# Kernel optimization log

Measured on AMD Instinct MI355X. Metric: run time of the kernel, lower is better.

The kernel has to match this reference:

```python
import jax, jax.numpy as jnp
import numpy as np

EMB = 1024
HID = 1024

def setup_inputs() -> dict:
    key = jax.random.key(0)
    k1, k2, k3, k4, k5 = jax.random.split(key, 5)
    s_ih = 1.0 / np.sqrt(HID)
    embeds = jax.random.normal(k1, (64, 512, EMB), dtype=jnp.float32)
    W_ih = jax.random.uniform(k2, (HID, EMB), jnp.float32, -s_ih, s_ih)
    W_hh = jax.random.uniform(k3, (HID, HID), jnp.float32, -s_ih, s_ih)
    b_ih = jax.random.uniform(k4, (HID,), jnp.float32, -s_ih, s_ih)
    b_hh = jax.random.uniform(k5, (HID,), jnp.float32, -s_ih, s_ih)
    return {"embeds": embeds, "W_ih": W_ih, "W_hh": W_hh, "b_ih": b_ih, "b_hh": b_hh}

def reference(embeds, W_ih, W_hh, b_ih, b_hh):
    # Elman RNN with tanh: h_t = tanh(x_t W_ih^T + b_ih + h_{t-1} W_hh^T + b_hh)
    B, S, _ = embeds.shape
    # Precompute input projection for all timesteps in one big GEMM: (B,S,H)
    x_proj = jnp.einsum('bse,he->bsh', embeds, W_ih) + b_ih + b_hh
    h0 = jnp.zeros((B, W_hh.shape[0]), dtype=embeds.dtype)

    def step(h, xp_t):
        h_new = jnp.tanh(xp_t + h @ W_hh.T)
        return h_new, h_new

    # scan over time axis: inputs (S,B,H)
    _, hs = jax.lax.scan(step, h0, jnp.swapaxes(x_proj, 0, 1))
    return hs  # (S, B, H): hidden state at each timestep
```

## Files before the change

kernel.cpp:

```cpp
#include <hip/hip_runtime.h>
#include <math.h>

#define EMB   1024
#define HID   1024
#define BATCH   64
#define SEQ    512

#define NBG    16
#define BTILE   4
#define NJT    16
#define JTILE  64

#define SLOT  65536

typedef float f32x4 __attribute__((ext_vector_type(4)));

__global__ __launch_bounds__(256) void xproj_gemm(
    const float* __restrict__ A,
    const float* __restrict__ W,
    const float* __restrict__ b_ih,
    const float* __restrict__ b_hh,
    float* __restrict__ out)
{
    __shared__ float As[16][68];
    __shared__ float Ws[16][68];

    const int tid = threadIdx.x;
    const int tx  = tid & 15;
    const int ty  = tid >> 4;
    const int m0  = blockIdx.y * 64;
    const int n0  = blockIdx.x * 64;
    const int lrow = tid >> 2;
    const int lk   = (tid & 3) * 4;

    float acc[4][4] = {};

    for (int kt = 0; kt < EMB; kt += 16) {
        float4 av = *(const float4*)&A[(size_t)(m0 + lrow) * EMB + kt + lk];
        float4 wv = *(const float4*)&W[(size_t)(n0 + lrow) * EMB + kt + lk];
        As[lk + 0][lrow] = av.x; As[lk + 1][lrow] = av.y;
        As[lk + 2][lrow] = av.z; As[lk + 3][lrow] = av.w;
        Ws[lk + 0][lrow] = wv.x; Ws[lk + 1][lrow] = wv.y;
        Ws[lk + 2][lrow] = wv.z; Ws[lk + 3][lrow] = wv.w;
        __syncthreads();
        #pragma unroll
        for (int kk = 0; kk < 16; ++kk) {
            float4 a = *(const float4*)&As[kk][ty * 4];
            float4 w = *(const float4*)&Ws[kk][tx * 4];
            acc[0][0] += a.x * w.x; acc[0][1] += a.x * w.y;
            acc[0][2] += a.x * w.z; acc[0][3] += a.x * w.w;
            acc[1][0] += a.y * w.x; acc[1][1] += a.y * w.y;
            acc[1][2] += a.y * w.z; acc[1][3] += a.y * w.w;
            acc[2][0] += a.z * w.x; acc[2][1] += a.z * w.y;
            acc[2][2] += a.z * w.z; acc[2][3] += a.z * w.w;
            acc[3][0] += a.w * w.x; acc[3][1] += a.w * w.y;
            acc[3][2] += a.w * w.z; acc[3][3] += a.w * w.w;
        }
        __syncthreads();
    }

    const int n = n0 + tx * 4;
    float bias[4];
    #pragma unroll
    for (int j = 0; j < 4; ++j) bias[j] = b_ih[n + j] + b_hh[n + j];

    #pragma unroll
    for (int i = 0; i < 4; ++i) {
        const int m = m0 + ty * 4 + i;
        const int b = m >> 9;
        const int s = m & 511;
        float4 o;
        o.x = acc[i][0] + bias[0];
        o.y = acc[i][1] + bias[1];
        o.z = acc[i][2] + bias[2];
        o.w = acc[i][3] + bias[3];
        *(float4*)&out[((size_t)(s * 64 + b) << 10) + n] = o;
    }
}

__device__ __forceinline__ float red16(float x) {
    int xi, yi;
    xi = __builtin_bit_cast(int, x);
    yi = __builtin_amdgcn_update_dpp(0, xi, 0xB1, 0xF, 0xF, true);
    x += __builtin_bit_cast(float, yi);
    xi = __builtin_bit_cast(int, x);
    yi = __builtin_amdgcn_update_dpp(0, xi, 0x4E, 0xF, 0xF, true);
    x += __builtin_bit_cast(float, yi);
    xi = __builtin_bit_cast(int, x);
    yi = __builtin_amdgcn_update_dpp(0, xi, 0x124, 0xF, 0xF, true);
    x += __builtin_bit_cast(float, yi);
    xi = __builtin_bit_cast(int, x);
    yi = __builtin_amdgcn_update_dpp(0, xi, 0x128, 0xF, 0xF, true);
    x += __builtin_bit_cast(float, yi);
    return x;
}

__device__ __forceinline__ f32x4 llc_load4_sync(const float* p) {
    f32x4 v;
    asm volatile("global_load_dwordx4 %0, %1, off sc1\n\t"
                 "s_waitcnt vmcnt(0)"
                 : "=&v"(v) : "v"(p) : "memory");
    return v;
}

__device__ __forceinline__ void llc_load4x2_sync(const float* p0, const float* p1,
                                                 f32x4& a, f32x4& b) {
    asm volatile("global_load_dwordx4 %0, %2, off sc1\n\t"
                 "global_load_dwordx4 %1, %3, off sc1\n\t"
                 "s_waitcnt vmcnt(0)"
                 : "=&v"(a), "=&v"(b) : "v"(p0), "v"(p1) : "memory");
}

__device__ __forceinline__ bool inrange4(f32x4 v, float lo, float hi) {
    return v.x >= lo && v.x <= hi && v.y >= lo && v.y <= hi &&
           v.z >= lo && v.z <= hi && v.w >= lo && v.w <= hi;
}

__global__ __launch_bounds__(512, 2) void rnn_persist(
    const float* __restrict__ Whh,
    float* __restrict__ out,
    float* __restrict__ exch)
{
    const int tid  = threadIdx.x;
    const int wave = tid >> 6;
    const int lane = tid & 63;
    const int c    = lane & 15;
    const int jp   = (lane >> 4) & 3;
    const int jt   = blockIdx.x;
    const int bg   = blockIdx.y;
    const int jbase = jt * JTILE + wave * 8 + jp * 2;
    const int k0    = c * 64;

    f32x4 wr0[16], wr1[16];
    #pragma unroll
    for (int kq = 0; kq < 16; ++kq) {
        wr0[kq] = *(const f32x4*)&Whh[(size_t)jbase * HID + k0 + kq * 4];
        wr1[kq] = *(const f32x4*)&Whh[(size_t)(jbase + 1) * HID + k0 + kq * 4];
    }
    #pragma unroll
    for (int kq = 0; kq < 16; ++kq) {
        asm volatile("" : "+v"(wr0[kq]));
        asm volatile("" : "+v"(wr1[kq]));
    }

    __shared__ float hsf[2 * 4352];

    const int p0 = tid, p1 = tid + 512;
    const int b0i = p0 >> 8, r0 = p0 & 255;
    const int b1i = p1 >> 8, r1 = p1 & 255;
    const int exoff0 = (bg * BTILE + b0i) * HID + r0 * 4;
    const int exoff1 = (bg * BTILE + b1i) * HID + r1 * 4;
    const int ldo0 = b0i * 1088 + (r0 >> 4) * 68 + (r0 & 15) * 4;
    const int ldo1 = b1i * 1088 + (r1 >> 4) * 68 + (r1 & 15) * 4;

    const int ob   = c >> 1;
    const int oidx = (bg * BTILE + ob) * HID + (jbase + (c & 1));

    if (c < 8) {
        float h0 = tanhf(out[oidx]);
        out[oidx] = h0;
        __hip_atomic_store(&exch[oidx], h0, __ATOMIC_RELAXED,
                           __HIP_MEMORY_SCOPE_AGENT);
    }

    for (int t = 1; t < SEQ; ++t) {
        float* cur = out + (size_t)t * (BATCH * HID);

        float xp = 0.f;
        if (c < 8) xp = cur[oidx];

        const float off = 4.0f * (float)((t - 1) & 3);
        const float lo  = off - 1.0f, hi = off + 1.0f;
        const float* eb = exch + ((t - 1) & 1) * SLOT;

        f32x4 v0, v1;
        llc_load4x2_sync(eb + exoff0, eb + exoff1, v0, v1);
        bool ok0 = inrange4(v0, lo, hi);
        bool ok1 = inrange4(v1, lo, hi);
        while (!__all(ok0 && ok1)) {
            __builtin_amdgcn_s_sleep(1);
            if (!ok0) { v0 = llc_load4_sync(eb + exoff0); ok0 = inrange4(v0, lo, hi); }
            if (!ok1) { v1 = llc_load4_sync(eb + exoff1); ok1 = inrange4(v1, lo, hi); }
        }
        v0 -= off;
        v1 -= off;

        const int bufb = (t & 1) * 4352;
        *(f32x4*)&hsf[bufb + ldo0] = v0;
        *(f32x4*)&hsf[bufb + ldo1] = v1;
        __syncthreads();

        float acc[4][2];
        #pragma unroll
        for (int b = 0; b < 4; ++b) {
            const f32x4* hb = (const f32x4*)&hsf[bufb + b * 1088 + c * 68];
            f32x4 s0 = {0.f, 0.f, 0.f, 0.f};
            f32x4 s1 = {0.f, 0.f, 0.f, 0.f};
            #pragma unroll
            for (int kq = 0; kq < 16; ++kq) {
                f32x4 h4 = hb[kq];
                s0 += h4 * wr0[kq];
                s1 += h4 * wr1[kq];
            }
            acc[b][0] = (s0.x + s0.y) + (s0.z + s0.w);
            acc[b][1] = (s1.x + s1.y) + (s1.z + s1.w);
        }

        #pragma unroll
        for (int b = 0; b < 4; ++b) {
            acc[b][0] = red16(acc[b][0]);
            acc[b][1] = red16(acc[b][1]);
        }

        float vb0 = (c & 1) ? acc[0][1] : acc[0][0];
        float vb1 = (c & 1) ? acc[1][1] : acc[1][0];
        float vb2 = (c & 1) ? acc[2][1] : acc[2][0];
        float vb3 = (c & 1) ? acc[3][1] : acc[3][0];
        float vlo = (c & 2) ? vb1 : vb0;
        float vhi = (c & 2) ? vb3 : vb2;
        float v   = (c & 4) ? vhi : vlo;
        if (c < 8) {
            float hv = tanhf(xp + v);
            cur[oidx] = hv;
            __hip_atomic_store(&exch[(t & 1) * SLOT + oidx],
                               hv + 4.0f * (float)(t & 3),
                               __ATOMIC_RELAXED, __HIP_MEMORY_SCOPE_AGENT);
        }
    }
}

extern "C" void kernel_launch(void* const* d_in, const int* in_sizes, int n_in,
                              void* d_out, int out_size, void* d_ws, size_t ws_size,
                              hipStream_t stream) {
    const float* embeds = (const float*)d_in[0];
    const float* W_ih   = (const float*)d_in[1];
    const float* W_hh   = (const float*)d_in[2];
    const float* b_ih   = (const float*)d_in[3];
    const float* b_hh   = (const float*)d_in[4];
    float* out = (float*)d_out;

    (void)in_sizes; (void)n_in; (void)out_size; (void)ws_size;

    hipMemsetAsync(d_ws, 0x7F, 2 * SLOT * sizeof(float), stream);

    dim3 gA(HID / 64, (BATCH * SEQ) / 64);
    xproj_gemm<<<gA, 256, 0, stream>>>(embeds, W_ih, b_ih, b_hh, out);

    dim3 gR(NJT, NBG);
    rnn_persist<<<gR, 512, 0, stream>>>(W_hh, out, (float*)d_ws);
}
```

Before: 2.574 ms.

## Pipeline RNN step per batch row with async prefetch of next hidden slice

The persistent RNN kernel now walks the four batch rows of each tile one at a time instead of gathering the whole 4x1024 hidden block before computing. Each row is published to the exchange buffer as soon as its tanh is done, one iteration late. The next row's exchange slice is prefetched asynchronously, so polling, compute and publishing overlap across batch rows and the critical cross-block dependency chain gets shorter. In exchange there are four barriers per timestep instead of one, and the ordering relies on hand-written waitcnt and barrier assembly. The final row of the last step is written out after the loop.

```diff
diff --git a/kernel.cpp b/kernel.cpp
--- a/kernel.cpp
+++ b/kernel.cpp
@@ -1,17 +1,18 @@
 #include <hip/hip_runtime.h>
 #include <math.h>
 
-#define EMB   1024
-#define HID   1024
-#define BATCH   64
-#define SEQ    512
-
-#define NBG    16
-#define BTILE   4
-#define NJT    16
-#define JTILE  64
-
-#define SLOT  65536
+#define EMB    1024
+#define HID    1024
+#define BATCH    64
+#define SEQ     512
+
+#define NBG     16
+#define BTILE    4
+#define NJT     16
+#define JTILE   64
+
+#define SLOT   65536
+#define STEPSZ 65536
 
 typedef float f32x4 __attribute__((ext_vector_type(4)));
 
@@ -95,6 +96,13 @@
     return x;
 }
 
+__device__ __forceinline__ f32x4 llc_load4_async(const float* p) {
+    f32x4 v;
+    asm volatile("global_load_dwordx4 %0, %1, off sc1"
+                 : "=&v"(v) : "v"(p) : "memory");
+    return v;
+}
+
 __device__ __forceinline__ f32x4 llc_load4_sync(const float* p) {
     f32x4 v;
     asm volatile("global_load_dwordx4 %0, %1, off sc1\n\t"
@@ -103,12 +111,13 @@
     return v;
 }
 
-__device__ __forceinline__ void llc_load4x2_sync(const float* p0, const float* p1,
-                                                 f32x4& a, f32x4& b) {
-    asm volatile("global_load_dwordx4 %0, %2, off sc1\n\t"
-                 "global_load_dwordx4 %1, %3, off sc1\n\t"
-                 "s_waitcnt vmcnt(0)"
-                 : "=&v"(a), "=&v"(b) : "v"(p0), "v"(p1) : "memory");
+__device__ __forceinline__ void wait_vm0() {
+    asm volatile("s_waitcnt vmcnt(0)" ::: "memory");
+    __builtin_amdgcn_sched_barrier(0);
+}
+
+__device__ __forceinline__ void bar_lgkm() {
+    asm volatile("s_waitcnt lgkmcnt(0)\n\ts_barrier" ::: "memory");
 }
 
 __device__ __forceinline__ bool inrange4(f32x4 v, float lo, float hi) {
@@ -125,10 +134,9 @@
     const int wave = tid >> 6;
     const int lane = tid & 63;
     const int c    = lane & 15;
-    const int jp   = (lane >> 4) & 3;
     const int jt   = blockIdx.x;
     const int bg   = blockIdx.y;
-    const int jbase = jt * JTILE + wave * 8 + jp * 2;
+    const int jbase = jt * JTILE + wave * 8 + ((lane >> 4) & 3) * 2;
     const int k0    = c * 64;
 
     f32x4 wr0[16], wr1[16];
@@ -143,89 +151,106 @@
         asm volatile("" : "+v"(wr1[kq]));
     }
 
-    __shared__ float hsf[2 * 4352];
-
-    const int p0 = tid, p1 = tid + 512;
-    const int b0i = p0 >> 8, r0 = p0 & 255;
-    const int b1i = p1 >> 8, r1 = p1 & 255;
-    const int exoff0 = (bg * BTILE + b0i) * HID + r0 * 4;
-    const int exoff1 = (bg * BTILE + b1i) * HID + r1 * 4;
-    const int ldo0 = b0i * 1088 + (r0 >> 4) * 68 + (r0 & 15) * 4;
-    const int ldo1 = b1i * 1088 + (r1 >> 4) * 68 + (r1 & 15) * 4;
-
-    const int ob   = c >> 1;
-    const int oidx = (bg * BTILE + ob) * HID + (jbase + (c & 1));
+    __shared__ float hsf[2 * 1088];
+
+    const bool have  = (tid < 256);
+    const int  fidx  = tid & 255;
+    const int  ldoff = (fidx >> 4) * 68 + (fidx & 15) * 4;
+    const int  gq    = fidx * 4;
+
+    const int jout  = jbase + (c & 1);
+    const int mybat = c >> 1;
+    const int orow  = (bg * BTILE + mybat) * HID + jout;
 
     if (c < 8) {
-        float h0 = tanhf(out[oidx]);
-        out[oidx] = h0;
-        __hip_atomic_store(&exch[oidx], h0, __ATOMIC_RELAXED,
+        float h0 = tanhf(out[orow]);
+        out[orow] = h0;
+        __hip_atomic_store(&exch[orow], h0, __ATOMIC_RELAXED,
                            __HIP_MEMORY_SCOPE_AGENT);
     }
 
+    float xp = 0.f;
+    if (c < 8) xp = out[(size_t)STEPSZ + orow];
+
+    f32x4 pf = {0.f, 0.f, 0.f, 0.f};
+    if (have) pf = llc_load4_async(exch + (bg * BTILE + 0) * HID + gq);
+
+    float pend = 0.f;
+
     for (int t = 1; t < SEQ; ++t) {
-        float* cur = out + (size_t)t * (BATCH * HID);
-
-        float xp = 0.f;
-        if (c < 8) xp = cur[oidx];
-
-        const float off = 4.0f * (float)((t - 1) & 3);
-        const float lo  = off - 1.0f, hi = off + 1.0f;
-        const float* eb = exch + ((t - 1) & 1) * SLOT;
-
-        f32x4 v0, v1;
-        llc_load4x2_sync(eb + exoff0, eb + exoff1, v0, v1);
-        bool ok0 = inrange4(v0, lo, hi);
-        bool ok1 = inrange4(v1, lo, hi);
-        while (!__all(ok0 && ok1)) {
-            __builtin_amdgcn_s_sleep(1);
-            if (!ok0) { v0 = llc_load4_sync(eb + exoff0); ok0 = inrange4(v0, lo, hi); }
-            if (!ok1) { v1 = llc_load4_sync(eb + exoff1); ok1 = inrange4(v1, lo, hi); }
-        }
-        v0 -= off;
-        v1 -= off;
-
-        const int bufb = (t & 1) * 4352;
-        *(f32x4*)&hsf[bufb + ldo0] = v0;
-        *(f32x4*)&hsf[bufb + ldo1] = v1;
-        __syncthreads();
-
-        float acc[4][2];
         #pragma unroll
         for (int b = 0; b < 4; ++b) {
-            const f32x4* hb = (const f32x4*)&hsf[bufb + b * 1088 + c * 68];
-            f32x4 s0 = {0.f, 0.f, 0.f, 0.f};
-            f32x4 s1 = {0.f, 0.f, 0.f, 0.f};
-            #pragma unroll
-            for (int kq = 0; kq < 16; ++kq) {
-                f32x4 h4 = hb[kq];
-                s0 += h4 * wr0[kq];
-                s1 += h4 * wr1[kq];
-            }
-            acc[b][0] = (s0.x + s0.y) + (s0.z + s0.w);
-            acc[b][1] = (s1.x + s1.y) + (s1.z + s1.w);
+            const int   tp    = t - 1;
+            const float off   = 4.0f * (float)(tp & 3);
+            const float lo    = off - 1.0f, hi = off + 1.0f;
+            const float* ebase = exch + (tp & 1) * SLOT + (bg * BTILE + b) * HID;
+
+            wait_vm0();
+
+            {
+                const int bprev = (b == 0) ? 3 : (b - 1);
+                const int tprev = (b == 0) ? (t - 1) : t;
+                if (!(b == 0 && t == 1)) {
+                    if (mybat == bprev) {
+                        const int oi = (bg * BTILE + bprev) * HID + jout;
+                        out[(size_t)tprev * STEPSZ + oi] = pend;
+                        __hip_atomic_store(&exch[(tprev & 1) * SLOT + oi],
+                                           pend + 4.0f * (float)(tprev & 3),
+                                           __ATOMIC_RELAXED,
+                                           __HIP_MEMORY_SCOPE_AGENT);
+                    }
+                }
+            }
+
+            bool ok = !have || inrange4(pf, lo, hi);
+            while (!__all(ok)) {
+                if (!ok) {
+                    pf = llc_load4_sync(ebase + gq);
+                    ok = inrange4(pf, lo, hi);
+                }
+            }
+
+            if (have) *(f32x4*)&hsf[(b & 1) * 1088 + ldoff] = pf - off;
+
+            {
+                const int bn = (b + 1) & 3;
+                const int tn = (b == 3) ? (t + 1) : t;
+                if (tn < SEQ) {
+                    const float* nb =
+                        exch + ((tn - 1) & 1) * SLOT + (bg * BTILE + bn) * HID;
+                    if (have) pf = llc_load4_async(nb + gq);
+                }
+            }
+
+            bar_lgkm();
+
+            {
+                const float* base = &hsf[(b & 1) * 1088 + c * 68];
+                f32x4 s0 = {0.f, 0.f, 0.f, 0.f};
+                f32x4 s1 = {0.f, 0.f, 0.f, 0.f};
+                #pragma unroll
+                for (int kq = 0; kq < 16; ++kq) {
+                    f32x4 h4 = *(const f32x4*)&base[kq * 4];
+                    s0 += h4 * wr0[kq];
+                    s1 += h4 * wr1[kq];
+                }
+                float a0 = (s0.x + s0.y) + (s0.z + s0.w);
+                float a1 = (s1.x + s1.y) + (s1.z + s1.w);
+                a0 = red16(a0);
+                a1 = red16(a1);
+                if (mybat == b) {
+                    pend = tanhf(xp + ((c & 1) ? a1 : a0));
+                }
+            }
+
+            if (b == 3 && t + 1 < SEQ) {
+                if (c < 8) xp = out[(size_t)(t + 1) * STEPSZ + orow];
+            }
         }
-
-        #pragma unroll
-        for (int b = 0; b < 4; ++b) {
-            acc[b][0] = red16(acc[b][0]);
-            acc[b][1] = red16(acc[b][1]);
-        }
-
-        float vb0 = (c & 1) ? acc[0][1] : acc[0][0];
-        float vb1 = (c & 1) ? acc[1][1] : acc[1][0];
-        float vb2 = (c & 1) ? acc[2][1] : acc[2][0];
-        float vb3 = (c & 1) ? acc[3][1] : acc[3][0];
-        float vlo = (c & 2) ? vb1 : vb0;
-        float vhi = (c & 2) ? vb3 : vb2;
-        float v   = (c & 4) ? vhi : vlo;
-        if (c < 8) {
-            float hv = tanhf(xp + v);
-            cur[oidx] = hv;
-            __hip_atomic_store(&exch[(t & 1) * SLOT + oidx],
-                               hv + 4.0f * (float)(t & 3),
-                               __ATOMIC_RELAXED, __HIP_MEMORY_SCOPE_AGENT);
-        }
+    }
+
+    if (mybat == 3) {
+        out[(size_t)(SEQ - 1) * STEPSZ + (bg * BTILE + 3) * HID + jout] = pend;
     }
 }
 
```

New measurement: 2.571 ms. Within noise of the previous version (-0.1%).

## Fuse input projection GEMM into persistent RNN kernel, overlapping with recurrence

Applied to the files above, without the earlier changes.

Removes the separate x-projection GEMM launch. Each persistent block now computes its own slice of the input projection: it precomputes the first 32 timesteps up front, then does one 64-wide K chunk per recurrent step to produce later timesteps ahead of use. The goal is to hide the GEMM work inside the latency-bound recurrence, where the block would otherwise idle waiting on the cross-block exchange. The cost is extra shared memory (about 70KB more per block), more instructions per step, and extra loads issued on the critical path.

```diff
diff --git a/kernel.cpp b/kernel.cpp
--- a/kernel.cpp
+++ b/kernel.cpp
@@ -1,82 +1,21 @@
 #include <hip/hip_runtime.h>
 #include <math.h>
 
-#define EMB   1024
-#define HID   1024
-#define BATCH   64
-#define SEQ    512
-
-#define NBG    16
-#define BTILE   4
-#define NJT    16
-#define JTILE  64
-
-#define SLOT  65536
+#define EMB    1024
+#define HID    1024
+#define BATCH    64
+#define SEQ     512
+
+#define NBG     16
+#define BTILE    4
+#define NJT     16
+#define JTILE   64
+
+#define SLOT   65536
+#define STEPSZ 65536
 
 typedef float f32x4 __attribute__((ext_vector_type(4)));
-
-__global__ __launch_bounds__(256) void xproj_gemm(
-    const float* __restrict__ A,
-    const float* __restrict__ W,
-    const float* __restrict__ b_ih,
-    const float* __restrict__ b_hh,
-    float* __restrict__ out)
-{
-    __shared__ float As[16][68];
-    __shared__ float Ws[16][68];
-
-    const int tid = threadIdx.x;
-    const int tx  = tid & 15;
-    const int ty  = tid >> 4;
-    const int m0  = blockIdx.y * 64;
-    const int n0  = blockIdx.x * 64;
-    const int lrow = tid >> 2;
-    const int lk   = (tid & 3) * 4;
-
-    float acc[4][4] = {};
-
-    for (int kt = 0; kt < EMB; kt += 16) {
-        float4 av = *(const float4*)&A[(size_t)(m0 + lrow) * EMB + kt + lk];
-        float4 wv = *(const float4*)&W[(size_t)(n0 + lrow) * EMB + kt + lk];
-        As[lk + 0][lrow] = av.x; As[lk + 1][lrow] = av.y;
-        As[lk + 2][lrow] = av.z; As[lk + 3][lrow] = av.w;
-        Ws[lk + 0][lrow] = wv.x; Ws[lk + 1][lrow] = wv.y;
-        Ws[lk + 2][lrow] = wv.z; Ws[lk + 3][lrow] = wv.w;
-        __syncthreads();
-        #pragma unroll
-        for (int kk = 0; kk < 16; ++kk) {
-            float4 a = *(const float4*)&As[kk][ty * 4];
-            float4 w = *(const float4*)&Ws[kk][tx * 4];
-            acc[0][0] += a.x * w.x; acc[0][1] += a.x * w.y;
-            acc[0][2] += a.x * w.z; acc[0][3] += a.x * w.w;
-            acc[1][0] += a.y * w.x; acc[1][1] += a.y * w.y;
-            acc[1][2] += a.y * w.z; acc[1][3] += a.y * w.w;
-            acc[2][0] += a.z * w.x; acc[2][1] += a.z * w.y;
-            acc[2][2] += a.z * w.z; acc[2][3] += a.z * w.w;
-            acc[3][0] += a.w * w.x; acc[3][1] += a.w * w.y;
-            acc[3][2] += a.w * w.z; acc[3][3] += a.w * w.w;
-        }
-        __syncthreads();
-    }
-
-    const int n = n0 + tx * 4;
-    float bias[4];
-    #pragma unroll
-    for (int j = 0; j < 4; ++j) bias[j] = b_ih[n + j] + b_hh[n + j];
-
-    #pragma unroll
-    for (int i = 0; i < 4; ++i) {
-        const int m = m0 + ty * 4 + i;
-        const int b = m >> 9;
-        const int s = m & 511;
-        float4 o;
-        o.x = acc[i][0] + bias[0];
-        o.y = acc[i][1] + bias[1];
-        o.z = acc[i][2] + bias[2];
-        o.w = acc[i][3] + bias[3];
-        *(float4*)&out[((size_t)(s * 64 + b) << 10) + n] = o;
-    }
-}
+typedef float f32x2 __attribute__((ext_vector_type(2)));
 
 __device__ __forceinline__ float red16(float x) {
     int xi, yi;
@@ -102,7 +41,6 @@
                  : "=&v"(v) : "v"(p) : "memory");
     return v;
 }
-
 __device__ __forceinline__ void llc_load4x2_sync(const float* p0, const float* p1,
                                                  f32x4& a, f32x4& b) {
     asm volatile("global_load_dwordx4 %0, %2, off sc1\n\t"
@@ -110,14 +48,17 @@
                  "s_waitcnt vmcnt(0)"
                  : "=&v"(a), "=&v"(b) : "v"(p0), "v"(p1) : "memory");
 }
-
 __device__ __forceinline__ bool inrange4(f32x4 v, float lo, float hi) {
     return v.x >= lo && v.x <= hi && v.y >= lo && v.y <= hi &&
            v.z >= lo && v.z <= hi && v.w >= lo && v.w <= hi;
 }
 
-__global__ __launch_bounds__(512, 2) void rnn_persist(
+__global__ __launch_bounds__(512, 2) void rnn_fused(
+    const float* __restrict__ embeds,
+    const float* __restrict__ W_ih,
     const float* __restrict__ Whh,
+    const float* __restrict__ b_ih,
+    const float* __restrict__ b_hh,
     float* __restrict__ out,
     float* __restrict__ exch)
 {
@@ -125,10 +66,9 @@
     const int wave = tid >> 6;
     const int lane = tid & 63;
     const int c    = lane & 15;
-    const int jp   = (lane >> 4) & 3;
     const int jt   = blockIdx.x;
     const int bg   = blockIdx.y;
-    const int jbase = jt * JTILE + wave * 8 + jp * 2;
+    const int jbase = jt * JTILE + wave * 8 + ((lane >> 4) & 3) * 2;
     const int k0    = c * 64;
 
     f32x4 wr0[16], wr1[16];
@@ -144,35 +84,106 @@
     }
 
     __shared__ float hsf[2 * 4352];
-
-    const int p0 = tid, p1 = tid + 512;
-    const int b0i = p0 >> 8, r0 = p0 & 255;
-    const int b1i = p1 >> 8, r1 = p1 & 255;
+    __shared__ float Axs[2][64][68];
+    __shared__ float Wxs[2][64][68];
+
+    const int b0i = tid >> 8,         r0 = tid & 255;
+    const int b1i = (tid + 512) >> 8, r1 = (tid + 512) & 255;
     const int exoff0 = (bg * BTILE + b0i) * HID + r0 * 4;
     const int exoff1 = (bg * BTILE + b1i) * HID + r1 * 4;
     const int ldo0 = b0i * 1088 + (r0 >> 4) * 68 + (r0 & 15) * 4;
     const int ldo1 = b1i * 1088 + (r1 >> 4) * 68 + (r1 & 15) * 4;
 
-    const int ob   = c >> 1;
-    const int oidx = (bg * BTILE + ob) * HID + (jbase + (c & 1));
+    const int jout  = jbase + (c & 1);
+    const int mybat = c >> 1;
+    const int orow  = (bg * BTILE + mybat) * HID + jout;
+
+    const int gty = tid >> 5;
+    const int gtx = tid & 31;
+    const int jx0 = jt * 64 + gtx * 2;
+    const float bias0 = b_ih[jx0] + b_hh[jx0];
+    const float bias1 = b_ih[jx0 + 1] + b_hh[jx0 + 1];
+    const int fm0 = (2 * tid) >> 4,     fk0 = (2 * tid) & 15;
+    const int fm1 = (2 * tid + 1) >> 4, fk1 = (2 * tid + 1) & 15;
+
+    f32x4 xaccA = {0.f,0.f,0.f,0.f};
+    f32x4 xaccB = {0.f,0.f,0.f,0.f};
+
+    auto xp_write = [&](int buf, f32x4 av0, f32x4 wv0, f32x4 av1, f32x4 wv1) {
+        Axs[buf][fk0*4+0][fm0]=av0.x; Axs[buf][fk0*4+1][fm0]=av0.y;
+        Axs[buf][fk0*4+2][fm0]=av0.z; Axs[buf][fk0*4+3][fm0]=av0.w;
+        Wxs[buf][fk0*4+0][fm0]=wv0.x; Wxs[buf][fk0*4+1][fm0]=wv0.y;
+        Wxs[buf][fk0*4+2][fm0]=wv0.z; Wxs[buf][fk0*4+3][fm0]=wv0.w;
+        Axs[buf][fk1*4+0][fm1]=av1.x; Axs[buf][fk1*4+1][fm1]=av1.y;
+        Axs[buf][fk1*4+2][fm1]=av1.z; Axs[buf][fk1*4+3][fm1]=av1.w;
+        Wxs[buf][fk1*4+0][fm1]=wv1.x; Wxs[buf][fk1*4+1][fm1]=wv1.y;
+        Wxs[buf][fk1*4+2][fm1]=wv1.z; Wxs[buf][fk1*4+3][fm1]=wv1.w;
+    };
+    auto xp_lda = [&](int sbase, int kc, int fm, int fk) -> f32x4 {
+        return *(const f32x4*)&embeds[
+            ((size_t)((bg*4 + (fm & 3)) * 512 + sbase + (fm >> 2)) << 10) + kc + fk*4];
+    };
+    auto xp_ldw = [&](int kc, int fm, int fk) -> f32x4 {
+        return *(const f32x4*)&W_ih[((size_t)(jt*64 + fm) << 10) + kc + fk*4];
+    };
+    auto xp_compute = [&](int buf) {
+        #pragma unroll
+        for (int kk = 0; kk < 64; ++kk) {
+            f32x4 a4 = *(const f32x4*)&Axs[buf][kk][gty * 4];
+            f32x2 w2 = *(const f32x2*)&Wxs[buf][kk][gtx * 2];
+            xaccA += a4 * w2.x;
+            xaccB += a4 * w2.y;
+        }
+    };
+    auto xp_store = [&](int sbase) {
+        float* o = &out[((size_t)((sbase + gty) * 64 + bg * 4) << 10) + jx0];
+        *(f32x2*)(o +    0) = f32x2{xaccA.x + bias0, xaccB.x + bias1};
+        *(f32x2*)(o + 1024) = f32x2{xaccA.y + bias0, xaccB.y + bias1};
+        *(f32x2*)(o + 2048) = f32x2{xaccA.z + bias0, xaccB.z + bias1};
+        *(f32x2*)(o + 3072) = f32x2{xaccA.w + bias0, xaccB.w + bias1};
+        xaccA = f32x4{0.f,0.f,0.f,0.f};
+        xaccB = f32x4{0.f,0.f,0.f,0.f};
+    };
+
+    for (int q = 0; q < 32; ++q) {
+        const int sb = (q >> 4) << 4;
+        const int kc = (q & 15) << 6;
+        xp_write(q & 1, xp_lda(sb, kc, fm0, fk0), xp_ldw(kc, fm0, fk0),
+                        xp_lda(sb, kc, fm1, fk1), xp_ldw(kc, fm1, fk1));
+        __syncthreads();
+        xp_compute(q & 1);
+        if ((q & 15) == 15) xp_store(sb);
+    }
+    __syncthreads();
 
     if (c < 8) {
-        float h0 = tanhf(out[oidx]);
-        out[oidx] = h0;
-        __hip_atomic_store(&exch[oidx], h0, __ATOMIC_RELAXED,
+        float h0 = tanhf(out[orow]);
+        out[orow] = h0;
+        __hip_atomic_store(&exch[orow], h0, __ATOMIC_RELAXED,
                            __HIP_MEMORY_SCOPE_AGENT);
     }
 
     for (int t = 1; t < SEQ; ++t) {
-        float* cur = out + (size_t)t * (BATCH * HID);
+        float* cur = out + (size_t)t * STEPSZ;
 
         float xp = 0.f;
-        if (c < 8) xp = cur[oidx];
+        if (c < 8) xp = cur[orow];
+
+        const bool doxp = (t <= 480);
+        const int  q    = t - 1;
+        const int  xbuf = q & 1;
+        const int  sb   = 32 + (q & ~15);
+        const int  kc   = (q & 15) << 6;
+        f32x4 av0, wv0, av1, wv1;
+        if (doxp) {
+            av0 = xp_lda(sb, kc, fm0, fk0); wv0 = xp_ldw(kc, fm0, fk0);
+            av1 = xp_lda(sb, kc, fm1, fk1); wv1 = xp_ldw(kc, fm1, fk1);
+            __builtin_amdgcn_sched_barrier(0);
+        }
 
         const float off = 4.0f * (float)((t - 1) & 3);
         const float lo  = off - 1.0f, hi = off + 1.0f;
         const float* eb = exch + ((t - 1) & 1) * SLOT;
-
         f32x4 v0, v1;
         llc_load4x2_sync(eb + exoff0, eb + exoff1, v0, v1);
         bool ok0 = inrange4(v0, lo, hi);
@@ -188,14 +199,14 @@
         const int bufb = (t & 1) * 4352;
         *(f32x4*)&hsf[bufb + ldo0] = v0;
         *(f32x4*)&hsf[bufb + ldo1] = v1;
+        if (doxp) xp_write(xbuf, av0, wv0, av1, wv1);
         __syncthreads();
 
         float acc[4][2];
         #pragma unroll
         for (int b = 0; b < 4; ++b) {
             const f32x4* hb = (const f32x4*)&hsf[bufb + b * 1088 + c * 68];
-            f32x4 s0 = {0.f, 0.f, 0.f, 0.f};
-            f32x4 s1 = {0.f, 0.f, 0.f, 0.f};
+            f32x4 s0 = {0.f,0.f,0.f,0.f}, s1 = {0.f,0.f,0.f,0.f};
             #pragma unroll
             for (int kq = 0; kq < 16; ++kq) {
                 f32x4 h4 = hb[kq];
@@ -205,13 +216,11 @@
             acc[b][0] = (s0.x + s0.y) + (s0.z + s0.w);
             acc[b][1] = (s1.x + s1.y) + (s1.z + s1.w);
         }
-
         #pragma unroll
         for (int b = 0; b < 4; ++b) {
             acc[b][0] = red16(acc[b][0]);
             acc[b][1] = red16(acc[b][1]);
         }
-
         float vb0 = (c & 1) ? acc[0][1] : acc[0][0];
         float vb1 = (c & 1) ? acc[1][1] : acc[1][0];
         float vb2 = (c & 1) ? acc[2][1] : acc[2][0];
@@ -221,10 +230,15 @@
         float v   = (c & 4) ? vhi : vlo;
         if (c < 8) {
             float hv = tanhf(xp + v);
-            cur[oidx] = hv;
-            __hip_atomic_store(&exch[(t & 1) * SLOT + oidx],
+            cur[orow] = hv;
+            __hip_atomic_store(&exch[(t & 1) * SLOT + orow],
                                hv + 4.0f * (float)(t & 3),
                                __ATOMIC_RELAXED, __HIP_MEMORY_SCOPE_AGENT);
+        }
+
+        if (doxp) {
+            xp_compute(xbuf);
+            if ((t & 15) == 0) xp_store(sb);
         }
     }
 }
@@ -241,11 +255,9 @@
 
     (void)in_sizes; (void)n_in; (void)out_size; (void)ws_size;
 
-    hipMemsetAsync(d_ws, 0x7F, 2 * SLOT * sizeof(float), stream);
-
-    dim3 gA(HID / 64, (BATCH * SEQ) / 64);
-    xproj_gemm<<<gA, 256, 0, stream>>>(embeds, W_ih, b_ih, b_hh, out);
+    hipMemsetAsync(d_ws, 0x7F, (size_t)2 * SLOT * sizeof(float), stream);
 
     dim3 gR(NJT, NBG);
-    rnn_persist<<<gR, 512, 0, stream>>>(W_hh, out, (float*)d_ws);
-}
+    rnn_fused<<<gR, 512, 0, stream>>>(embeds, W_ih, W_hh, b_ih, b_hh,
+                                      out, (float*)d_ws);
+}
```

Result: no change. 2.539 ms (-1.3%).
